# Kernel optimization log

Hardware: AMD Instinct MI355X
Metric: run time of the kernel (lower is better)

The kernel has to match this reference:

```python
import jax, jax.numpy as jnp
import numpy as np

N_NODES = 20000
N_EDGES = 320000
IN_CH = 512
HID = 128
HEADS = 4
OUT_CH = 256
NEG_SLOPE = 0.2


def _gat_layer(x, edge_index, W, a_src, a_dst, bias, heads, out_ch, concat):
    """PyG GATConv (add_self_loops=True, eval mode: no dropout).
    x: [N, F_in], edge_index: [2, E] (row 0 = src, row 1 = dst).
    Returns (out, alpha) with alpha: [E+N, heads].
    """
    N = x.shape[0]
    h = (x @ W).reshape(N, heads, out_ch)                      # [N, H, C]
    loops = jnp.arange(N, dtype=edge_index.dtype)
    src = jnp.concatenate([edge_index[0], loops])
    dst = jnp.concatenate([edge_index[1], loops])
    a_s = jnp.einsum('nhc,hc->nh', h, a_src)                   # [N, H]
    a_d = jnp.einsum('nhc,hc->nh', h, a_dst)
    e = a_s[src] + a_d[dst]                                    # [E', H]
    e = jnp.where(e > 0, e, NEG_SLOPE * e)                     # LeakyReLU
    # segment softmax over incoming edges of each dst node
    emax = jax.ops.segment_max(e, dst, num_segments=N)
    ex = jnp.exp(e - emax[dst])
    denom = jax.ops.segment_sum(ex, dst, num_segments=N)
    alpha = ex / denom[dst]                                    # [E', H]
    msg = alpha[:, :, None] * h[src]                           # [E', H, C]
    out = jax.ops.segment_sum(msg, dst, num_segments=N)        # [N, H, C]
    out = out.reshape(N, heads * out_ch) if concat else out.mean(axis=1)
    return out + bias, alpha


def setup_inputs() -> dict:
    key = jax.random.key(0)
    ks = jax.random.split(key, 10)
    s = 0.05
    x = jax.random.normal(ks[0], (N_NODES, IN_CH), dtype=jnp.float32)
    edge_index = jax.random.randint(ks[1], (2, N_EDGES), 0, N_NODES, dtype=jnp.int32)
    W1 = jax.random.normal(ks[2], (IN_CH, HEADS * HID), dtype=jnp.float32) * s
    a_src1 = jax.random.normal(ks[3], (HEADS, HID), dtype=jnp.float32) * s
    a_dst1 = jax.random.normal(ks[4], (HEADS, HID), dtype=jnp.float32) * s
    b1 = jnp.zeros((HEADS * HID,), dtype=jnp.float32)
    W2 = jax.random.normal(ks[5], (HEADS * HID, OUT_CH), dtype=jnp.float32) * s
    a_src2 = jax.random.normal(ks[6], (1, OUT_CH), dtype=jnp.float32) * s
    a_dst2 = jax.random.normal(ks[7], (1, OUT_CH), dtype=jnp.float32) * s
    b2 = jnp.zeros((OUT_CH,), dtype=jnp.float32)
    return {"x": x, "edge_index": edge_index, "W1": W1, "a_src1": a_src1,
            "a_dst1": a_dst1, "b1": b1, "W2": W2, "a_src2": a_src2,
            "a_dst2": a_dst2, "b2": b2}


def reference(x, edge_index, W1, a_src1, a_dst1, b1, W2, a_src2, a_dst2, b2):
    h, alpha1 = _gat_layer(x, edge_index, W1, a_src1, a_dst1, b1, HEADS, HID, True)
    h = jax.nn.elu(h)
    # dropout inactive in eval mode
    out, alpha2 = _gat_layer(h, edge_index, W2, a_src2, a_dst2, b2, 1, OUT_CH, False)
    return out, alpha1, alpha2
```

## Files before the change

kernel.cpp:

```cpp
#include <hip/hip_runtime.h>
#include <hip/hip_bf16.h>
#include <cstdint>


#define NNODES 20000
#define NEDGES 320000
#define ETOT   340000
#define F1     512
#define F2     256
#define HEADS  4

typedef __bf16 bf16;
typedef __attribute__((ext_vector_type(8))) __bf16 bf16x8;
typedef __attribute__((ext_vector_type(4))) float f32x4;

__device__ __forceinline__ void gload_lds16(const void* g, void* l) {
    __builtin_amdgcn_global_load_lds(
        (const __attribute__((address_space(1))) void*)g,
        (__attribute__((address_space(3))) void*)l, 16, 0, 0);
}

__global__ void deg_count(const int* __restrict__ ei, int* __restrict__ deg) {
    int e = blockIdx.x * blockDim.x + threadIdx.x;
    if (e >= ETOT) return;
    int dst = (e < NEDGES) ? ei[NEDGES + e] : (e - NEDGES);
    atomicAdd(&deg[dst], 1);
}

__global__ void scan_deg(const int* __restrict__ deg, int* __restrict__ offs,
                         int* __restrict__ cur) {
    __shared__ int sums[1024];
    const int t = threadIdx.x;
    const int PER = 20;
    int base = t * PER;
    int local[PER];
    int run = 0;
#pragma unroll
    for (int j = 0; j < PER; j++) {
        int i = base + j;
        int v = (i < NNODES) ? deg[i] : 0;
        local[j] = run;
        run += v;
    }
    sums[t] = run;
    __syncthreads();
    for (int o = 1; o < 1024; o <<= 1) {
        int v = (t >= o) ? sums[t - o] : 0;
        __syncthreads();
        sums[t] += v;
        __syncthreads();
    }
    int texcl = (t == 0) ? 0 : sums[t - 1];
#pragma unroll
    for (int j = 0; j < PER; j++) {
        int i = base + j;
        if (i < NNODES) {
            int e = texcl + local[j];
            cur[i] = e;
            offs[i] = e;
        }
    }
    if (t == 1023) offs[NNODES] = sums[1023];
}

__global__ void fill_csr(const int* __restrict__ ei, int* __restrict__ cur,
                         int* __restrict__ csr_src, int* __restrict__ csr_eid) {
    int e = blockIdx.x * blockDim.x + threadIdx.x;
    if (e >= ETOT) return;
    int src, dst;
    if (e < NEDGES) { src = ei[e]; dst = ei[NEDGES + e]; }
    else            { src = dst = e - NEDGES; }
    int p = atomicAdd(&cur[dst], 1);
    csr_src[p] = src;
    csr_eid[p] = e;
}

__device__ __forceinline__ void swz(const float* __restrict__ W, bf16* __restrict__ Wh,
                                    bf16* __restrict__ Wl, int N, int idx) {
    int lane = idx & 63;
    int tile = idx >> 6;
    int NT = N >> 4;
    int kt = tile / NT, nt = tile - kt * NT;
    int krow = kt * 32 + (lane >> 4) * 8;
    int col  = nt * 16 + (lane & 15);
    union { bf16 b[8]; uint4 u; } hi, lo;
#pragma unroll
    for (int j = 0; j < 8; j++) {
        float w = W[(size_t)(krow + j) * N + col];
        bf16 h = (bf16)w;
        hi.b[j] = h;
        lo.b[j] = (bf16)(w - (float)h);
    }
    *(uint4*)(Wh + (size_t)idx * 8) = hi.u;
    *(uint4*)(Wl + (size_t)idx * 8) = lo.u;
}

__global__ void swizzle_both(const float* __restrict__ W1, bf16* __restrict__ W1h,
                             bf16* __restrict__ W1l, const float* __restrict__ W2,
                             bf16* __restrict__ W2h, bf16* __restrict__ W2l) {
    int idx = blockIdx.x * blockDim.x + threadIdx.x;
    const int t1 = (512 * 512) >> 3;
    const int t2 = (512 * 256) >> 3;
    if (idx < t1) swz(W1, W1h, W1l, 512, idx);
    else if (idx < t1 + t2) swz(W2, W2h, W2l, 256, idx - t1);
}

template <int K, int N, bool ASPLIT>
__global__ __launch_bounds__(256) void gemm_fused(const float* __restrict__ A,
                                                  const bf16* __restrict__ Ah,
                                                  const bf16* __restrict__ Al,
                                                  const bf16* __restrict__ Bh,
                                                  const bf16* __restrict__ Bl,
                                                  bf16* __restrict__ Cb,
                                                  const float* __restrict__ asrc,
                                                  const float* __restrict__ adst,
                                                  float* __restrict__ as_out,
                                                  float* __restrict__ ad_out, int M) {
    __shared__ __align__(16) char smem[2][16384];
    const int lane = threadIdx.x & 63;
    const int wave = threadIdx.x >> 6;
    const int row_base = blockIdx.x * 64 + wave * 16;
    const int colt0 = blockIdx.y * 8;
    constexpr int NT = N / 16;

    const char* hbase = (const char*)Bh + (size_t)colt0 * 1024;
    const char* lbase = (const char*)Bl + (size_t)colt0 * 1024;
    auto stage = [&](int kt, int buf) {
        size_t kb = (size_t)kt * NT * 1024;
#pragma unroll
        for (int q = 0; q < 4; q++) {
            int off = wave * 4096 + q * 1024;
            const char* src = (off < 8192) ? (hbase + kb + off)
                                           : (lbase + kb + (off - 8192));
            gload_lds16(src + lane * 16, &smem[buf][off]);
        }
    };

    int r0 = row_base + (lane & 15);
    if (r0 >= M) r0 = M - 1;
    const float* aptr = A ? (A + (size_t)r0 * K + ((lane >> 4) * 8)) : nullptr;
    const bf16* ahp = ASPLIT ? (Ah + (size_t)r0 * K + ((lane >> 4) * 8)) : nullptr;
    const bf16* alp = ASPLIT ? (Al + (size_t)r0 * K + ((lane >> 4) * 8)) : nullptr;

    float4 nf0, nf1;
    bf16x8 nah, nal;
    auto fetchA = [&](int kt) {
        if constexpr (ASPLIT) {
            nah = *(const bf16x8*)(ahp + kt * 32);
            nal = *(const bf16x8*)(alp + kt * 32);
        } else {
            nf0 = *(const float4*)(aptr + kt * 32);
            nf1 = *(const float4*)(aptr + kt * 32 + 4);
        }
    };
    bf16x8 cah, cal;
    auto cvtA = [&]() {
        if constexpr (ASPLIT) {
            cah = nah;
            cal = nal;
        } else {
            float av[8];
            *(float4*)(av)     = nf0;
            *(float4*)(av + 4) = nf1;
#pragma unroll
            for (int j = 0; j < 8; j++) {
                bf16 h = (bf16)av[j];
                cah[j] = h;
                cal[j] = (bf16)(av[j] - (float)h);
            }
        }
    };

    f32x4 acc[8] = {};
    stage(0, 0);
    fetchA(0);
    __syncthreads();
    for (int kt = 0; kt < K / 32; ++kt) {
        cvtA();
        if (kt + 1 < K / 32) {
            stage(kt + 1, (kt + 1) & 1);
            fetchA(kt + 1);
        }
        const char* bb = smem[kt & 1];
#pragma unroll
        for (int c = 0; c < 8; c++) {
            bf16x8 bh = *(const bf16x8*)(bb + c * 1024 + lane * 16);
            bf16x8 bl = *(const bf16x8*)(bb + 8192 + c * 1024 + lane * 16);
            acc[c] = __builtin_amdgcn_mfma_f32_16x16x32_bf16(cah, bh, acc[c], 0, 0, 0);
            acc[c] = __builtin_amdgcn_mfma_f32_16x16x32_bf16(cah, bl, acc[c], 0, 0, 0);
            acc[c] = __builtin_amdgcn_mfma_f32_16x16x32_bf16(cal, bh, acc[c], 0, 0, 0);
        }
        __syncthreads();
    }

    const int crow0 = row_base + (lane >> 4) * 4;
    const int col15 = lane & 15;
#pragma unroll
    for (int c = 0; c < 8; c++)
#pragma unroll
        for (int r = 0; r < 4; r++) {
            int rr = crow0 + r;
            if (rr < M)
                Cb[(size_t)rr * N + (colt0 + c) * 16 + col15] = (bf16)acc[c][r];
        }

    float ss[4] = {}, sd[4] = {};
#pragma unroll
    for (int c = 0; c < 8; c++) {
        int cw = blockIdx.y * 128 + c * 16 + col15;
        float was = asrc[cw];
        float wad = adst[cw];
#pragma unroll
        for (int r = 0; r < 4; r++) {
            ss[r] += acc[c][r] * was;
            sd[r] += acc[c][r] * wad;
        }
    }
#pragma unroll
    for (int o = 1; o < 16; o <<= 1)
#pragma unroll
        for (int r = 0; r < 4; r++) {
            ss[r] += __shfl_xor(ss[r], o);
            sd[r] += __shfl_xor(sd[r], o);
        }
    if (col15 == 0) {
#pragma unroll
        for (int r = 0; r < 4; r++) {
            int rr = crow0 + r;
            if (rr < M) {
                if constexpr (N == 512) {
                    as_out[rr * 4 + blockIdx.y] = ss[r];
                    ad_out[rr * 4 + blockIdx.y] = sd[r];
                } else {
                    atomicAdd(&as_out[rr], ss[r]);
                    atomicAdd(&ad_out[rr], sd[r]);
                }
            }
        }
    }
}

__global__ __launch_bounds__(256) void alpha1k(const float* __restrict__ as1,
                                               const float* __restrict__ ad1,
                                               const int* __restrict__ offs,
                                               const int* __restrict__ csrS,
                                               const int* __restrict__ csrE,
                                               float* __restrict__ alpha1,
                                               float* __restrict__ aC1) {
    int n = blockIdx.x * 4 + (threadIdx.x >> 6);
    int lane = threadIdx.x & 63;
    if (n >= NNODES) return;
    int beg = offs[n], deg = offs[n + 1] - beg;

    float4 ad4 = *(const float4*)(ad1 + n * 4);
    const float adn[4] = {ad4.x, ad4.y, ad4.z, ad4.w};

    float v0[4] = {};
    int e0 = 0;
    float mx[4] = {-3e38f, -3e38f, -3e38f, -3e38f};
    for (int idx = lane; idx < deg; idx += 64) {
        int s = csrS[beg + idx];
        float4 a4 = *(const float4*)(as1 + s * 4);
        float v[4] = {a4.x + adn[0], a4.y + adn[1], a4.z + adn[2], a4.w + adn[3]};
#pragma unroll
        for (int k = 0; k < 4; k++) {
            v[k] = v[k] > 0.f ? v[k] : 0.2f * v[k];
            mx[k] = fmaxf(mx[k], v[k]);
        }
        if (idx == lane) {
            e0 = csrE[beg + idx];
#pragma unroll
            for (int k = 0; k < 4; k++) v0[k] = v[k];
        }
    }
#pragma unroll
    for (int o = 1; o < 64; o <<= 1)
#pragma unroll
        for (int k = 0; k < 4; k++) mx[k] = fmaxf(mx[k], __shfl_xor(mx[k], o));

    float ex0[4] = {0.f, 0.f, 0.f, 0.f};
    float ls[4] = {0.f, 0.f, 0.f, 0.f};
    if (lane < deg) {
#pragma unroll
        for (int k = 0; k < 4; k++) { ex0[k] = __expf(v0[k] - mx[k]); ls[k] = ex0[k]; }
    }
    for (int idx = lane + 64; idx < deg; idx += 64) {
        int s = csrS[beg + idx];
        float4 a4 = *(const float4*)(as1 + s * 4);
        float v[4] = {a4.x + adn[0], a4.y + adn[1], a4.z + adn[2], a4.w + adn[3]};
#pragma unroll
        for (int k = 0; k < 4; k++) {
            v[k] = v[k] > 0.f ? v[k] : 0.2f * v[k];
            ls[k] += __expf(v[k] - mx[k]);
        }
    }
#pragma unroll
    for (int o = 1; o < 64; o <<= 1)
#pragma unroll
        for (int k = 0; k < 4; k++) ls[k] += __shfl_xor(ls[k], o);
    float rden[4];
#pragma unroll
    for (int k = 0; k < 4; k++) rden[k] = 1.f / ls[k];

    for (int idx = lane; idx < deg; idx += 64) {
        float al[4];
        int e;
        if (idx == lane) {
            e = e0;
#pragma unroll
            for (int k = 0; k < 4; k++) al[k] = ex0[k] * rden[k];
        } else {
            int s = csrS[beg + idx];
            e = csrE[beg + idx];
            float4 a4 = *(const float4*)(as1 + s * 4);
            float v[4] = {a4.x + adn[0], a4.y + adn[1], a4.z + adn[2], a4.w + adn[3]};
#pragma unroll
            for (int k = 0; k < 4; k++) {
                v[k] = v[k] > 0.f ? v[k] : 0.2f * v[k];
                al[k] = __expf(v[k] - mx[k]) * rden[k];
            }
        }
        float4 f = make_float4(al[0], al[1], al[2], al[3]);
        *(float4*)(aC1 + (size_t)(beg + idx) * 4) = f;
        *(float4*)(alpha1 + (size_t)e * 4) = f;
    }
}

__global__ __launch_bounds__(256) void alpha2k(const float* __restrict__ as2,
                                               const float* __restrict__ ad2,
                                               const int* __restrict__ offs,
                                               const int* __restrict__ csrS,
                                               const int* __restrict__ csrE,
                                               float* __restrict__ alpha2,
                                               float* __restrict__ aC2) {
    int n = blockIdx.x * 4 + (threadIdx.x >> 6);
    int lane = threadIdx.x & 63;
    if (n >= NNODES) return;
    int beg = offs[n], deg = offs[n + 1] - beg;
    const float adn = ad2[n];

    float v0 = 0.f;
    int e0 = 0;
    float mx = -3e38f;
    for (int idx = lane; idx < deg; idx += 64) {
        int s = csrS[beg + idx];
        float v = as2[s] + adn;
        v = v > 0.f ? v : 0.2f * v;
        mx = fmaxf(mx, v);
        if (idx == lane) { e0 = csrE[beg + idx]; v0 = v; }
    }
#pragma unroll
    for (int o = 1; o < 64; o <<= 1) mx = fmaxf(mx, __shfl_xor(mx, o));

    float ex0 = 0.f, ls = 0.f;
    if (lane < deg) { ex0 = __expf(v0 - mx); ls = ex0; }
    for (int idx = lane + 64; idx < deg; idx += 64) {
        int s = csrS[beg + idx];
        float v = as2[s] + adn;
        v = v > 0.f ? v : 0.2f * v;
        ls += __expf(v - mx);
    }
#pragma unroll
    for (int o = 1; o < 64; o <<= 1) ls += __shfl_xor(ls, o);
    float rden = 1.f / ls;

    for (int idx = lane; idx < deg; idx += 64) {
        float a;
        int e;
        if (idx == lane) { e = e0; a = ex0 * rden; }
        else {
            int s = csrS[beg + idx];
            e = csrE[beg + idx];
            float v = as2[s] + adn;
            v = v > 0.f ? v : 0.2f * v;
            a = __expf(v - mx) * rden;
        }
        aC2[beg + idx] = a;
        alpha2[e] = a;
    }
}

__global__ __launch_bounds__(64) void agg1(const bf16* __restrict__ h1b,
                                           const float* __restrict__ aC1,
                                           const int* __restrict__ offs,
                                           const int* __restrict__ csrS,
                                           const float* __restrict__ b1,
                                           bf16* __restrict__ h1eh,
                                           bf16* __restrict__ h1el) {
    const int n = blockIdx.x >> 3, cq = blockIdx.x & 7;
    const int lane = threadIdx.x;
    const int h = cq >> 1;
    const int beg = offs[n];
    const int deg = offs[n + 1] - beg;
    const int ch = (cq << 6) + lane;
    const bf16* __restrict__ hb = h1b + ch;

    float acc = 0.f;
#pragma unroll 4
    for (int i = 0; i < deg; ++i) {
        int s = csrS[beg + i];
        float a = aC1[(size_t)(beg + i) * 4 + h];
        acc += a * (float)hb[(size_t)s * F1];
    }
    float t = acc + b1[ch];
    t = t > 0.f ? t : expm1f(t);
    bf16 hi = (bf16)t;
    h1eh[(size_t)n * F1 + ch] = hi;
    h1el[(size_t)n * F1 + ch] = (bf16)(t - (float)hi);
}

__global__ __launch_bounds__(64) void agg2(const bf16* __restrict__ h2b,
                                           const float* __restrict__ aC2,
                                           const int* __restrict__ offs,
                                           const int* __restrict__ csrS,
                                           const float* __restrict__ b2,
                                           float* __restrict__ out) {
    const int n = blockIdx.x >> 2, cq = blockIdx.x & 3;
    const int lane = threadIdx.x;
    const int beg = offs[n];
    const int deg = offs[n + 1] - beg;
    const int ch = (cq << 6) + lane;
    const bf16* __restrict__ hb = h2b + ch;

    float acc = 0.f;
#pragma unroll 4
    for (int i = 0; i < deg; ++i) {
        int s = csrS[beg + i];
        float a = aC2[beg + i];
        acc += a * (float)hb[(size_t)s * F2];
    }
    out[(size_t)n * F2 + ch] = acc + b2[ch];
}

extern "C" void kernel_launch(void* const* d_in, const int* in_sizes, int n_in,
                              void* d_out, int out_size, void* d_ws, size_t ws_size,
                              hipStream_t stream) {
    const float* x      = (const float*)d_in[0];
    const int*   ei     = (const int*)d_in[1];
    const float* W1     = (const float*)d_in[2];
    const float* a_src1 = (const float*)d_in[3];
    const float* a_dst1 = (const float*)d_in[4];
    const float* b1     = (const float*)d_in[5];
    const float* W2     = (const float*)d_in[6];
    const float* a_src2 = (const float*)d_in[7];
    const float* a_dst2 = (const float*)d_in[8];
    const float* b2     = (const float*)d_in[9];

    char* ws = (char*)d_ws;
    size_t off = 0;
    auto alloc = [&](size_t bytes) -> char* {
        char* p = ws + off;
        off += (bytes + 255) & ~(size_t)255;
        return p;
    };
    bf16*  h1b  = (bf16*) alloc((size_t)NNODES * F1 * 2);
    bf16*  h2b  = (bf16*) alloc((size_t)NNODES * F2 * 2);
    bf16*  h1eh = (bf16*) alloc((size_t)NNODES * F1 * 2);
    bf16*  h1el = (bf16*) alloc((size_t)NNODES * F1 * 2);
    float* aC1  = (float*)alloc((size_t)ETOT * 4 * 4);
    float* aC2  = (float*)alloc((size_t)ETOT * 4);
    float* as1  = (float*)alloc((size_t)NNODES * 4 * 4);
    float* ad1  = (float*)alloc((size_t)NNODES * 4 * 4);
    int*   deg  = (int*)  alloc((size_t)NNODES * 4);
    float* as2  = (float*)alloc((size_t)NNODES * 4);
    float* ad2  = (float*)alloc((size_t)NNODES * 4);
    bf16*  W1h  = (bf16*) alloc((size_t)512 * 512 * 2);
    bf16*  W1l  = (bf16*) alloc((size_t)512 * 512 * 2);
    bf16*  W2h  = (bf16*) alloc((size_t)512 * 256 * 2);
    bf16*  W2l  = (bf16*) alloc((size_t)512 * 256 * 2);
    int*   offs = (int*)  alloc((size_t)(NNODES + 1) * 4);
    int*   cur  = (int*)  alloc((size_t)NNODES * 4);
    int*   csrS = (int*)  alloc((size_t)ETOT * 4);
    int*   csrE = (int*)  alloc((size_t)ETOT * 4);

    float* out2   = (float*)d_out;
    float* alpha1 = out2 + (size_t)NNODES * F2;
    float* alpha2 = alpha1 + (size_t)ETOT * HEADS;

    hipMemsetAsync(deg, 0, (size_t)((char*)ad2 - (char*)deg) + NNODES * 4, stream);
    deg_count<<<(ETOT + 255) / 256, 256, 0, stream>>>(ei, deg);
    scan_deg<<<1, 1024, 0, stream>>>(deg, offs, cur);
    fill_csr<<<(ETOT + 255) / 256, 256, 0, stream>>>(ei, cur, csrS, csrE);

    swizzle_both<<<(49152 + 255) / 256, 256, 0, stream>>>(W1, W1h, W1l, W2, W2h, W2l);

    gemm_fused<512, 512, false><<<dim3(313, 4), 256, 0, stream>>>(
        x, nullptr, nullptr, W1h, W1l, h1b, a_src1, a_dst1, as1, ad1, NNODES);
    alpha1k<<<(NNODES + 3) / 4, 256, 0, stream>>>(as1, ad1, offs, csrS, csrE,
                                                  alpha1, aC1);
    agg1<<<NNODES * 8, 64, 0, stream>>>(h1b, aC1, offs, csrS, b1, h1eh, h1el);

    gemm_fused<512, 256, true><<<dim3(313, 2), 256, 0, stream>>>(
        nullptr, h1eh, h1el, W2h, W2l, h2b, a_src2, a_dst2, as2, ad2, NNODES);
    alpha2k<<<(NNODES + 3) / 4, 256, 0, stream>>>(as2, ad2, offs, csrS, csrE,
                                                  alpha2, aC2);
    agg2<<<NNODES * 4, 64, 0, stream>>>(h2b, aC2, offs, csrS, b2, out2);
}
```

Baseline: 363.1 us.

## Split layer-2 GEMM into smaller-tile kernel and batch gather loads in aggregation

Replaces the templated GEMM with a dedicated layer-1 kernel and a new layer-2 kernel. The layer-2 kernel uses 32-row tiles with waves split across column halves, which doubles the block count for the 256-wide output to improve occupancy. Both aggregation kernels now pack four nodes per 256-thread block and issue eight neighbour index, weight and feature loads at a time before accumulating, to raise memory-level parallelism on the gathers. Row bounds checks were dropped in gemm2, which relies on the node count dividing evenly into 32-row tiles.

```diff
diff --git a/kernel.cpp b/kernel.cpp
--- a/kernel.cpp
+++ b/kernel.cpp
@@ -105,23 +105,20 @@
     else if (idx < t1 + t2) swz(W2, W2h, W2l, 256, idx - t1);
 }
 
-template <int K, int N, bool ASPLIT>
-__global__ __launch_bounds__(256) void gemm_fused(const float* __restrict__ A,
-                                                  const bf16* __restrict__ Ah,
-                                                  const bf16* __restrict__ Al,
-                                                  const bf16* __restrict__ Bh,
-                                                  const bf16* __restrict__ Bl,
-                                                  bf16* __restrict__ Cb,
-                                                  const float* __restrict__ asrc,
-                                                  const float* __restrict__ adst,
-                                                  float* __restrict__ as_out,
-                                                  float* __restrict__ ad_out, int M) {
+__global__ __launch_bounds__(256) void gemm1(const float* __restrict__ A,
+                                             const bf16* __restrict__ Bh,
+                                             const bf16* __restrict__ Bl,
+                                             bf16* __restrict__ Cb,
+                                             const float* __restrict__ asrc,
+                                             const float* __restrict__ adst,
+                                             float* __restrict__ as_out,
+                                             float* __restrict__ ad_out, int M) {
+    constexpr int K = 512, N = 512, NT = N / 16;
     __shared__ __align__(16) char smem[2][16384];
     const int lane = threadIdx.x & 63;
     const int wave = threadIdx.x >> 6;
     const int row_base = blockIdx.x * 64 + wave * 16;
     const int colt0 = blockIdx.y * 8;
-    constexpr int NT = N / 16;
 
     const char* hbase = (const char*)Bh + (size_t)colt0 * 1024;
     const char* lbase = (const char*)Bl + (size_t)colt0 * 1024;
@@ -138,36 +135,23 @@
 
     int r0 = row_base + (lane & 15);
     if (r0 >= M) r0 = M - 1;
-    const float* aptr = A ? (A + (size_t)r0 * K + ((lane >> 4) * 8)) : nullptr;
-    const bf16* ahp = ASPLIT ? (Ah + (size_t)r0 * K + ((lane >> 4) * 8)) : nullptr;
-    const bf16* alp = ASPLIT ? (Al + (size_t)r0 * K + ((lane >> 4) * 8)) : nullptr;
+    const float* aptr = A + (size_t)r0 * K + ((lane >> 4) * 8);
 
     float4 nf0, nf1;
-    bf16x8 nah, nal;
     auto fetchA = [&](int kt) {
-        if constexpr (ASPLIT) {
-            nah = *(const bf16x8*)(ahp + kt * 32);
-            nal = *(const bf16x8*)(alp + kt * 32);
-        } else {
-            nf0 = *(const float4*)(aptr + kt * 32);
-            nf1 = *(const float4*)(aptr + kt * 32 + 4);
-        }
+        nf0 = *(const float4*)(aptr + kt * 32);
+        nf1 = *(const float4*)(aptr + kt * 32 + 4);
     };
     bf16x8 cah, cal;
     auto cvtA = [&]() {
-        if constexpr (ASPLIT) {
-            cah = nah;
-            cal = nal;
-        } else {
-            float av[8];
-            *(float4*)(av)     = nf0;
-            *(float4*)(av + 4) = nf1;
-#pragma unroll
-            for (int j = 0; j < 8; j++) {
-                bf16 h = (bf16)av[j];
-                cah[j] = h;
-                cal[j] = (bf16)(av[j] - (float)h);
-            }
+        float av[8];
+        *(float4*)(av)     = nf0;
+        *(float4*)(av + 4) = nf1;
+#pragma unroll
+        for (int j = 0; j < 8; j++) {
+            bf16 h = (bf16)av[j];
+            cah[j] = h;
+            cal[j] = (bf16)(av[j] - (float)h);
         }
     };
 
@@ -228,14 +212,111 @@
         for (int r = 0; r < 4; r++) {
             int rr = crow0 + r;
             if (rr < M) {
-                if constexpr (N == 512) {
-                    as_out[rr * 4 + blockIdx.y] = ss[r];
-                    ad_out[rr * 4 + blockIdx.y] = sd[r];
-                } else {
-                    atomicAdd(&as_out[rr], ss[r]);
-                    atomicAdd(&ad_out[rr], sd[r]);
-                }
+                as_out[rr * 4 + blockIdx.y] = ss[r];
+                ad_out[rr * 4 + blockIdx.y] = sd[r];
             }
+        }
+    }
+}
+
+__global__ __launch_bounds__(256) void gemm2(const bf16* __restrict__ Ah,
+                                             const bf16* __restrict__ Al,
+                                             const bf16* __restrict__ Bh,
+                                             const bf16* __restrict__ Bl,
+                                             bf16* __restrict__ Cb,
+                                             const float* __restrict__ asrc,
+                                             const float* __restrict__ adst,
+                                             float* __restrict__ as_out,
+                                             float* __restrict__ ad_out) {
+    constexpr int K = 512, N = 256, NT = N / 16;
+    __shared__ __align__(16) char smem[2][16384];
+    const int lane = threadIdx.x & 63;
+    const int wave = threadIdx.x >> 6;
+    const int rowt = wave >> 1, colh = wave & 1;
+    const int row_base = blockIdx.x * 32 + rowt * 16;
+    const int colt0 = blockIdx.y * 8;
+
+    const char* hbase = (const char*)Bh + (size_t)colt0 * 1024;
+    const char* lbase = (const char*)Bl + (size_t)colt0 * 1024;
+    auto stage = [&](int kt, int buf) {
+        size_t kb = (size_t)kt * NT * 1024;
+#pragma unroll
+        for (int q = 0; q < 4; q++) {
+            int off = wave * 4096 + q * 1024;
+            const char* src = (off < 8192) ? (hbase + kb + off)
+                                           : (lbase + kb + (off - 8192));
+            gload_lds16(src + lane * 16, &smem[buf][off]);
+        }
+    };
+
+    int r0 = row_base + (lane & 15);
+    const bf16* ahp = Ah + (size_t)r0 * K + ((lane >> 4) * 8);
+    const bf16* alp = Al + (size_t)r0 * K + ((lane >> 4) * 8);
+
+    bf16x8 nah, nal, cah, cal;
+    auto fetchA = [&](int kt) {
+        nah = *(const bf16x8*)(ahp + kt * 32);
+        nal = *(const bf16x8*)(alp + kt * 32);
+    };
+
+    f32x4 acc[4] = {};
+    stage(0, 0);
+    fetchA(0);
+    __syncthreads();
+    for (int kt = 0; kt < K / 32; ++kt) {
+        cah = nah; cal = nal;
+        if (kt + 1 < K / 32) {
+            stage(kt + 1, (kt + 1) & 1);
+            fetchA(kt + 1);
+        }
+        const char* bb = smem[kt & 1];
+#pragma unroll
+        for (int c = 0; c < 4; c++) {
+            int ct = colh * 4 + c;
+            bf16x8 bh = *(const bf16x8*)(bb + ct * 1024 + lane * 16);
+            bf16x8 bl = *(const bf16x8*)(bb + 8192 + ct * 1024 + lane * 16);
+            acc[c] = __builtin_amdgcn_mfma_f32_16x16x32_bf16(cah, bh, acc[c], 0, 0, 0);
+            acc[c] = __builtin_amdgcn_mfma_f32_16x16x32_bf16(cah, bl, acc[c], 0, 0, 0);
+            acc[c] = __builtin_amdgcn_mfma_f32_16x16x32_bf16(cal, bh, acc[c], 0, 0, 0);
+        }
+        __syncthreads();
+    }
+
+    const int crow0 = row_base + (lane >> 4) * 4;
+    const int col15 = lane & 15;
+#pragma unroll
+    for (int c = 0; c < 4; c++)
+#pragma unroll
+        for (int r = 0; r < 4; r++) {
+            int rr = crow0 + r;
+            Cb[(size_t)rr * N + (colt0 + colh * 4 + c) * 16 + col15] = (bf16)acc[c][r];
+        }
+
+    float ss[4] = {}, sd[4] = {};
+#pragma unroll
+    for (int c = 0; c < 4; c++) {
+        int cw = blockIdx.y * 128 + (colh * 4 + c) * 16 + col15;
+        float was = asrc[cw];
+        float wad = adst[cw];
+#pragma unroll
+        for (int r = 0; r < 4; r++) {
+            ss[r] += acc[c][r] * was;
+            sd[r] += acc[c][r] * wad;
+        }
+    }
+#pragma unroll
+    for (int o = 1; o < 16; o <<= 1)
+#pragma unroll
+        for (int r = 0; r < 4; r++) {
+            ss[r] += __shfl_xor(ss[r], o);
+            sd[r] += __shfl_xor(sd[r], o);
+        }
+    if (col15 == 0) {
+#pragma unroll
+        for (int r = 0; r < 4; r++) {
+            int rr = crow0 + r;
+            atomicAdd(&as_out[rr], ss[r]);
+            atomicAdd(&ad_out[rr], sd[r]);
         }
     }
 }
@@ -380,15 +461,16 @@
     }
 }
 
-__global__ __launch_bounds__(64) void agg1(const bf16* __restrict__ h1b,
-                                           const float* __restrict__ aC1,
-                                           const int* __restrict__ offs,
-                                           const int* __restrict__ csrS,
-                                           const float* __restrict__ b1,
-                                           bf16* __restrict__ h1eh,
-                                           bf16* __restrict__ h1el) {
-    const int n = blockIdx.x >> 3, cq = blockIdx.x & 7;
-    const int lane = threadIdx.x;
+__global__ __launch_bounds__(256) void agg1(const bf16* __restrict__ h1b,
+                                            const float* __restrict__ aC1,
+                                            const int* __restrict__ offs,
+                                            const int* __restrict__ csrS,
+                                            const float* __restrict__ b1,
+                                            bf16* __restrict__ h1eh,
+                                            bf16* __restrict__ h1el) {
+    const int group = blockIdx.x >> 3, cq = blockIdx.x & 7;
+    const int wave = threadIdx.x >> 6, lane = threadIdx.x & 63;
+    const int n = group * 4 + wave;
     const int h = cq >> 1;
     const int beg = offs[n];
     const int deg = offs[n + 1] - beg;
@@ -396,8 +478,24 @@
     const bf16* __restrict__ hb = h1b + ch;
 
     float acc = 0.f;
-#pragma unroll 4
-    for (int i = 0; i < deg; ++i) {
+    int i = 0;
+    for (; i + 8 <= deg; i += 8) {
+        int   sarr[8];
+        float aarr[8];
+        float hv[8];
+#pragma unroll
+        for (int j = 0; j < 8; j++) {
+            sarr[j] = csrS[beg + i + j];
+            aarr[j] = aC1[(size_t)(beg + i + j) * 4 + h];
+        }
+#pragma unroll
+        for (int j = 0; j < 8; j++)
+            hv[j] = (float)hb[(size_t)sarr[j] * F1];
+#pragma unroll
+        for (int j = 0; j < 8; j++)
+            acc += aarr[j] * hv[j];
+    }
+    for (; i < deg; ++i) {
         int s = csrS[beg + i];
         float a = aC1[(size_t)(beg + i) * 4 + h];
         acc += a * (float)hb[(size_t)s * F1];
@@ -409,22 +507,39 @@
     h1el[(size_t)n * F1 + ch] = (bf16)(t - (float)hi);
 }
 
-__global__ __launch_bounds__(64) void agg2(const bf16* __restrict__ h2b,
-                                           const float* __restrict__ aC2,
-                                           const int* __restrict__ offs,
-                                           const int* __restrict__ csrS,
-                                           const float* __restrict__ b2,
-                                           float* __restrict__ out) {
-    const int n = blockIdx.x >> 2, cq = blockIdx.x & 3;
-    const int lane = threadIdx.x;
+__global__ __launch_bounds__(256) void agg2(const bf16* __restrict__ h2b,
+                                            const float* __restrict__ aC2,
+                                            const int* __restrict__ offs,
+                                            const int* __restrict__ csrS,
+                                            const float* __restrict__ b2,
+                                            float* __restrict__ out) {
+    const int group = blockIdx.x >> 2, cq = blockIdx.x & 3;
+    const int wave = threadIdx.x >> 6, lane = threadIdx.x & 63;
+    const int n = group * 4 + wave;
     const int beg = offs[n];
     const int deg = offs[n + 1] - beg;
     const int ch = (cq << 6) + lane;
     const bf16* __restrict__ hb = h2b + ch;
 
     float acc = 0.f;
-#pragma unroll 4
-    for (int i = 0; i < deg; ++i) {
+    int i = 0;
+    for (; i + 8 <= deg; i += 8) {
+        int   sarr[8];
+        float aarr[8];
+        float hv[8];
+#pragma unroll
+        for (int j = 0; j < 8; j++) {
+            sarr[j] = csrS[beg + i + j];
+            aarr[j] = aC2[beg + i + j];
+        }
+#pragma unroll
+        for (int j = 0; j < 8; j++)
+            hv[j] = (float)hb[(size_t)sarr[j] * F2];
+#pragma unroll
+        for (int j = 0; j < 8; j++)
+            acc += aarr[j] * hv[j];
+    }
+    for (; i < deg; ++i) {
         int s = csrS[beg + i];
         float a = aC2[beg + i];
         acc += a * (float)hb[(size_t)s * F2];
@@ -484,15 +599,15 @@
 
     swizzle_both<<<(49152 + 255) / 256, 256, 0, stream>>>(W1, W1h, W1l, W2, W2h, W2l);
 
-    gemm_fused<512, 512, false><<<dim3(313, 4), 256, 0, stream>>>(
-        x, nullptr, nullptr, W1h, W1l, h1b, a_src1, a_dst1, as1, ad1, NNODES);
+    gemm1<<<dim3(313, 4), 256, 0, stream>>>(
+        x, W1h, W1l, h1b, a_src1, a_dst1, as1, ad1, NNODES);
     alpha1k<<<(NNODES + 3) / 4, 256, 0, stream>>>(as1, ad1, offs, csrS, csrE,
                                                   alpha1, aC1);
-    agg1<<<NNODES * 8, 64, 0, stream>>>(h1b, aC1, offs, csrS, b1, h1eh, h1el);
-
-    gemm_fused<512, 256, true><<<dim3(313, 2), 256, 0, stream>>>(
-        nullptr, h1eh, h1el, W2h, W2l, h2b, a_src2, a_dst2, as2, ad2, NNODES);
+    agg1<<<5000 * 8, 256, 0, stream>>>(h1b, aC1, offs, csrS, b1, h1eh, h1el);
+
+    gemm2<<<dim3(625, 2), 256, 0, stream>>>(
+        h1eh, h1el, W2h, W2l, h2b, a_src2, a_dst2, as2, ad2);
     alpha2k<<<(NNODES + 3) / 4, 256, 0, stream>>>(as2, ad2, offs, csrS, csrE,
                                                   alpha2, aC2);
-    agg2<<<NNODES * 4, 64, 0, stream>>>(h2b, aC2, offs, csrS, b2, out2);
-}
+    agg2<<<5000 * 4, 256, 0, stream>>>(h2b, aC2, offs, csrS, b2, out2);
+}
```

Measured after the change: 410.4 us. +13.0%, slower.
